# Kernel optimization log

Hardware: AMD Instinct MI355X
Metric: run time of the kernel (lower is better)

The kernel has to match this reference:

```python
import jax, jax.numpy as jnp
import numpy as np

EPS = 1e-5
G = 8    # groups
K = 3    # kernel_size


def bn(x, gamma, beta, mean, var):
    # inference-mode BatchNorm2d; x: (b,C,H,W), params: (C,)
    inv = gamma / jnp.sqrt(var + EPS)
    return x * inv[None, :, None, None] + (beta - mean * inv)[None, :, None, None]


def gconv1x1(x, w):
    # grouped 1x1 conv; x: (b, g*ci, H, W), w: (g, co, ci) -> (b, g*co, H, W)
    b, C, H, W = x.shape
    g, co, ci = w.shape
    xg = x.reshape(b, g, ci, H, W)
    y = jnp.einsum('bgihw,goi->bgohw', xg, w)
    return y.reshape(b, g * co, H, W)


def unfold3(x):
    # torch.nn.Unfold(k=3, stride=1, dilation=1, padding=1), reshaped to (b, C, 9, H, W)
    b, C, H, W = x.shape
    xp = jnp.pad(x, ((0, 0), (0, 0), (1, 1), (1, 1)))
    patches = [xp[:, :, i:i + H, j:j + W] for i in range(K) for j in range(K)]
    return jnp.stack(patches, axis=2)


def setup_inputs() -> dict:
    key = jax.random.key(0)
    ks = jax.random.split(key, 16)
    f = jax.random.normal
    u = jax.random.uniform
    return {
        'x':  f(ks[0], (2, 256, 128, 128), jnp.float32),
        'w1': f(ks[1], (8, 8, 32), jnp.float32) * 0.1,
        'b1': f(ks[2], (64,), jnp.float32) * 0.1,
        'g1': u(ks[3], (64,), jnp.float32, 0.5, 1.5),
        'be1': f(ks[4], (64,), jnp.float32) * 0.1,
        'm1': f(ks[5], (64,), jnp.float32) * 0.1,
        'v1': u(ks[6], (64,), jnp.float32, 0.5, 1.5),
        'w2': f(ks[7], (8, 10, 8), jnp.float32) * 0.1,
        'b2': f(ks[8], (80,), jnp.float32) * 0.1,
        'g2': u(ks[9], (80,), jnp.float32, 0.5, 1.5),
        'be2': f(ks[10], (80,), jnp.float32) * 0.1,
        'm2': f(ks[11], (80,), jnp.float32) * 0.1,
        'v2': u(ks[12], (80,), jnp.float32, 0.5, 1.5),
        'wv': f(ks[13], (8, 32, 32), jnp.float32) * 0.1,
    }


def reference(x, w1, b1, g1, be1, m1, v1, w2, b2, g2, be2, m2, v2, wv):
    b, C, H, W = x.shape
    # mask_conv: grouped 1x1 conv -> BN -> tanh -> grouped 1x1 conv -> BN
    t = jnp.tanh(bn(gconv1x1(x, w1) + b1[None, :, None, None], g1, be1, m1, v1))
    mn = bn(gconv1x1(t, w2) + b2[None, :, None, None], g2, be2, m2, v2)  # (b, G*(1+K*K), H, W)
    neighbor = mn[:, :G]          # (b, G, H, W)
    mask = mn[:, G:]              # (b, G*K*K, H, W)
    nb = unfold3(neighbor)        # (b, G, 9, H, W)
    logits = mask.reshape(b, G, K * K, H, W) + nb
    attn = jax.nn.softmax(logits, axis=2)               # (b, G, 9, H, W)
    # value path: grouped 1x1 conv (no bias) then unfold
    v = gconv1x1(x, wv)                                  # (b, C, H, W)
    vu = unfold3(v).reshape(b, G, C // G, K * K, H, W)   # (b, G, C/G, 9, H, W)
    out = jnp.einsum('bgkhw,bgckhw->bgchw', attn, vu)    # weighted sum over window
    return out.reshape(b, C, H, W)
```

## Files before the change

kernel.cpp:

```cpp
#include <hip/hip_runtime.h>

#define HW  16384
#define WD  128

#define TS   16
#define HS   18
#define HP   (HS * HS)
#define PRS  20
#define PLS  360

__device__ __forceinline__ unsigned short f2bf(float f) {
    unsigned int u = __builtin_bit_cast(unsigned int, f);
    u += 0x7FFFu + ((u >> 16) & 1u);
    return (unsigned short)(u >> 16);
}
__device__ __forceinline__ float bf2f(unsigned int s) {
    return __builtin_bit_cast(float, (s & 0xFFFFu) << 16);
}
__device__ __forceinline__ float ftanh(float v) {
    const float e = __expf(2.0f * v);
    return 1.0f - __fdividef(2.0f, e + 1.0f);
}

__global__ __launch_bounds__(256) void la_t(
    const float* __restrict__ x,
    const float* __restrict__ w1, const float* __restrict__ b1,
    const float* __restrict__ g1, const float* __restrict__ be1,
    const float* __restrict__ m1, const float* __restrict__ v1,
    ushort4* __restrict__ t4, uint4* __restrict__ xbf)
{
    const int z   = blockIdx.x;
    const int b   = blockIdx.y;
    const int pix = blockIdx.z * blockDim.x + threadIdx.x;
    const int p   = z & 7;
    const int h   = z >> 3;

    const float* xp = x + (size_t)(b * 256 + p * 32) * HW + pix;
    float xv[32];
#pragma unroll
    for (int c = 0; c < 32; ++c) xv[c] = xp[(size_t)c * HW];

#pragma unroll
    for (int j = 0; j < 2; ++j) {
        const int c8 = h * 2 + j;
        uint4 u;
        u.x = (unsigned)f2bf(xv[c8 * 8 + 0]) | ((unsigned)f2bf(xv[c8 * 8 + 1]) << 16);
        u.y = (unsigned)f2bf(xv[c8 * 8 + 2]) | ((unsigned)f2bf(xv[c8 * 8 + 3]) << 16);
        u.z = (unsigned)f2bf(xv[c8 * 8 + 4]) | ((unsigned)f2bf(xv[c8 * 8 + 5]) << 16);
        u.w = (unsigned)f2bf(xv[c8 * 8 + 6]) | ((unsigned)f2bf(xv[c8 * 8 + 7]) << 16);
        xbf[((size_t)((b * 8 + p) * 4 + c8)) * HW + pix] = u;
    }

    const float* w1g = w1 + p * 256 + h * 4 * 32;
    float tv[4];
#pragma unroll
    for (int o = 0; o < 4; ++o) {
        float a = 0.f;
#pragma unroll
        for (int ci = 0; ci < 32; ++ci) a = fmaf(xv[ci], w1g[o * 32 + ci], a);
        const int ch = p * 8 + h * 4 + o;
        const float inv = g1[ch] * rsqrtf(v1[ch] + 1e-5f);
        const float add = be1[ch] + (b1[ch] - m1[ch]) * inv;
        tv[o] = ftanh(fmaf(a, inv, add));
    }

    t4[((size_t)((b * 8 + p) * 2 + h)) * HW + pix] =
        make_ushort4(f2bf(tv[0]), f2bf(tv[1]), f2bf(tv[2]), f2bf(tv[3]));
}

__global__ __launch_bounds__(256, 4) void la_fused(
    const float* __restrict__ w2, const float* __restrict__ b2,
    const float* __restrict__ g2, const float* __restrict__ be2,
    const float* __restrict__ m2, const float* __restrict__ v2,
    const float* __restrict__ wv,
    const ushort4* __restrict__ t4, const uint4* __restrict__ xbf,
    float* __restrict__ out)
{
    __shared__ uint4 xt[4 * PLS];
    __shared__ float nbs[PLS];

    const int tid  = threadIdx.x;
    const int bg   = blockIdx.x;
    const int tile = blockIdx.y;
    const int b    = bg >> 3, g = bg & 7;
    const int ty0  = (tile >> 3) * TS;
    const int tx0  = (tile & 7) * TS;

    const uint4*   xg = xbf + (size_t)((b * 8 + g) * 4) * HW;
    const ushort4* t0 = t4  + (size_t)(b * 16) * HW;

    const int cy  = tid >> 4, cx = tid & 15;
    const int ciy = ty0 + cy, cix = tx0 + cx;
    const int cpx = ciy * WD + cix;

    const int mc0    = 8 + 9 * g;
    const int pa     = mc0 / 10;
    const int pb     = (mc0 + 8) / 10;
    const int ksplit = 10 - (mc0 - pa * 10);

    const ushort4 tAlo = t4[((size_t)((b * 8 + pa) * 2 + 0)) * HW + cpx];
    const ushort4 tAhi = t4[((size_t)((b * 8 + pa) * 2 + 1)) * HW + cpx];
    const ushort4 tBlo = t4[((size_t)((b * 8 + pb) * 2 + 0)) * HW + cpx];
    const ushort4 tBhi = t4[((size_t)((b * 8 + pb) * 2 + 1)) * HW + cpx];

    const float inv2n = g2[g] * rsqrtf(v2[g] + 1e-5f);
    const float add2n = be2[g] + (b2[g] - m2[g]) * inv2n;

    for (int hp = tid; hp < HP; hp += 256) {
        const int hy = hp / HS, hx = hp - hy * HS;
        const int iy = ty0 + hy - 1, ix = tx0 + hx - 1;
        const int slot = hy * PRS + hx;
        if (((unsigned)iy < 128u) && ((unsigned)ix < 128u)) {
            const int po = iy * WD + ix;
            const ushort4 ta = t0[po];
            const ushort4 tb = t0[(size_t)HW + po];
            float an = 0.f;
            an = fmaf(bf2f(ta.x), w2[g * 8 + 0], an);
            an = fmaf(bf2f(ta.y), w2[g * 8 + 1], an);
            an = fmaf(bf2f(ta.z), w2[g * 8 + 2], an);
            an = fmaf(bf2f(ta.w), w2[g * 8 + 3], an);
            an = fmaf(bf2f(tb.x), w2[g * 8 + 4], an);
            an = fmaf(bf2f(tb.y), w2[g * 8 + 5], an);
            an = fmaf(bf2f(tb.z), w2[g * 8 + 6], an);
            an = fmaf(bf2f(tb.w), w2[g * 8 + 7], an);
            nbs[slot] = fmaf(an, inv2n, add2n);
#pragma unroll
            for (int c8 = 0; c8 < 4; ++c8)
                xt[c8 * PLS + slot] = xg[(size_t)c8 * HW + po];
        } else {
            const uint4 z = make_uint4(0u, 0u, 0u, 0u);
#pragma unroll
            for (int c8 = 0; c8 < 4; ++c8) xt[c8 * PLS + slot] = z;
            nbs[slot] = 0.f;
        }
    }
    __syncthreads();

    float tA[8], tB[8];
    tA[0] = bf2f(tAlo.x); tA[1] = bf2f(tAlo.y);
    tA[2] = bf2f(tAlo.z); tA[3] = bf2f(tAlo.w);
    tA[4] = bf2f(tAhi.x); tA[5] = bf2f(tAhi.y);
    tA[6] = bf2f(tAhi.z); tA[7] = bf2f(tAhi.w);
    tB[0] = bf2f(tBlo.x); tB[1] = bf2f(tBlo.y);
    tB[2] = bf2f(tBlo.z); tB[3] = bf2f(tBlo.w);
    tB[4] = bf2f(tBhi.x); tB[5] = bf2f(tBhi.y);
    tB[6] = bf2f(tBhi.z); tB[7] = bf2f(tBhi.w);

    float lg[9];
    float mx = -1e30f;
#pragma unroll
    for (int k = 0; k < 9; ++k) {
        const int mc = mc0 + k;
        const int p  = (k < ksplit) ? pa : pb;
        const int o  = mc - p * 10;
        const float* w2p = w2 + p * 80 + o * 8;
        float a = 0.f;
#pragma unroll
        for (int i = 0; i < 8; ++i) {
            const float ti = (k < ksplit) ? tA[i] : tB[i];
            a = fmaf(ti, w2p[i], a);
        }
        const float inv = g2[mc] * rsqrtf(v2[mc] + 1e-5f);
        const float add = be2[mc] + (b2[mc] - m2[mc]) * inv;
        lg[k] = fmaf(a, inv, add) + nbs[(cy + k / 3) * PRS + (cx + k % 3)];
        mx = fmaxf(mx, lg[k]);
    }
    float ssum = 0.f;
#pragma unroll
    for (int k = 0; k < 9; ++k) { lg[k] = __expf(lg[k] - mx); ssum += lg[k]; }
    const float rs = 1.f / ssum;

    float s[32];
#pragma unroll
    for (int c = 0; c < 32; ++c) s[c] = 0.f;
#pragma unroll
    for (int k = 0; k < 9; ++k) {
        const int slot = (cy + k / 3) * PRS + (cx + k % 3);
        const float e = lg[k];
#pragma unroll
        for (int c8 = 0; c8 < 4; ++c8) {
            const uint4 u = xt[c8 * PLS + slot];
            s[c8 * 8 + 0] = fmaf(e, bf2f(u.x),       s[c8 * 8 + 0]);
            s[c8 * 8 + 1] = fmaf(e, bf2f(u.x >> 16), s[c8 * 8 + 1]);
            s[c8 * 8 + 2] = fmaf(e, bf2f(u.y),       s[c8 * 8 + 2]);
            s[c8 * 8 + 3] = fmaf(e, bf2f(u.y >> 16), s[c8 * 8 + 3]);
            s[c8 * 8 + 4] = fmaf(e, bf2f(u.z),       s[c8 * 8 + 4]);
            s[c8 * 8 + 5] = fmaf(e, bf2f(u.z >> 16), s[c8 * 8 + 5]);
            s[c8 * 8 + 6] = fmaf(e, bf2f(u.w),       s[c8 * 8 + 6]);
            s[c8 * 8 + 7] = fmaf(e, bf2f(u.w >> 16), s[c8 * 8 + 7]);
        }
    }

    const float* wvg = wv + g * 1024;
    float* og = out + (size_t)(b * 256 + g * 32) * HW + cpx;
#pragma unroll 4
    for (int o = 0; o < 32; ++o) {
        const float* wp = wvg + o * 32;
        float a = 0.f;
#pragma unroll
        for (int ci = 0; ci < 32; ++ci) a = fmaf(s[ci], wp[ci], a);
        __builtin_nontemporal_store(a * rs, og + (size_t)o * HW);
    }
}

extern "C" void kernel_launch(void* const* d_in, const int* in_sizes, int n_in,
                              void* d_out, int out_size, void* d_ws, size_t ws_size,
                              hipStream_t stream)
{
    const float* x   = (const float*)d_in[0];
    const float* w1  = (const float*)d_in[1];
    const float* b1  = (const float*)d_in[2];
    const float* g1  = (const float*)d_in[3];
    const float* be1 = (const float*)d_in[4];
    const float* m1  = (const float*)d_in[5];
    const float* v1  = (const float*)d_in[6];
    const float* w2  = (const float*)d_in[7];
    const float* b2  = (const float*)d_in[8];
    const float* g2  = (const float*)d_in[9];
    const float* be2 = (const float*)d_in[10];
    const float* m2  = (const float*)d_in[11];
    const float* v2  = (const float*)d_in[12];
    const float* wv  = (const float*)d_in[13];

    float* out = (float*)d_out;
    ushort4* t4  = (ushort4*)d_ws;
    uint4*   xbf = (uint4*)((char*)d_ws + (size_t)32 * HW * 8);

    dim3 blk(256);
    dim3 gt(16, 2, HW / 256);
    dim3 gfd(16, 64);

    hipLaunchKernelGGL(la_t, gt, blk, 0, stream,
                       x, w1, b1, g1, be1, m1, v1, t4, xbf);
    hipLaunchKernelGGL(la_fused, gfd, blk, 0, stream,
                       w2, b2, g2, be2, m2, v2, wv, t4, xbf, out);
}
```

Before: 129.3 us.

## Compute value projection with bf16 MFMA via shared-memory staged aggregates

```diff
diff --git a/kernel.cpp b/kernel.cpp
--- a/kernel.cpp
+++ b/kernel.cpp
@@ -8,6 +8,10 @@
 #define HP   (HS * HS)
 #define PRS  20
 #define PLS  360
+#define SROW 80
+
+typedef __attribute__((ext_vector_type(8))) short bf16x8;
+typedef __attribute__((ext_vector_type(4))) float f32x4;
 
 __device__ __forceinline__ unsigned short f2bf(float f) {
     unsigned int u = __builtin_bit_cast(unsigned int, f);
@@ -68,7 +72,7 @@
         make_ushort4(f2bf(tv[0]), f2bf(tv[1]), f2bf(tv[2]), f2bf(tv[3]));
 }
 
-__global__ __launch_bounds__(256, 4) void la_fused(
+__global__ __launch_bounds__(256) void la_fused(
     const float* __restrict__ w2, const float* __restrict__ b2,
     const float* __restrict__ g2, const float* __restrict__ be2,
     const float* __restrict__ m2, const float* __restrict__ v2,
@@ -85,13 +89,24 @@
     const int b    = bg >> 3, g = bg & 7;
     const int ty0  = (tile >> 3) * TS;
     const int tx0  = (tile & 7) * TS;
+    const int lane = tid & 63, wv4 = tid >> 6;
 
     const uint4*   xg = xbf + (size_t)((b * 8 + g) * 4) * HW;
     const ushort4* t0 = t4  + (size_t)(b * 16) * HW;
 
+    const float* wvg = wv + g * 1024;
+    bf16x8 bfrag[2];
+#pragma unroll
+    for (int nt = 0; nt < 2; ++nt) {
+        const float* wp = wvg + (nt * 16 + (lane & 15)) * 32 + (lane >> 4) * 8;
+        bf16x8 f;
+#pragma unroll
+        for (int j = 0; j < 8; ++j) f[j] = (short)f2bf(wp[j]);
+        bfrag[nt] = f;
+    }
+
     const int cy  = tid >> 4, cx = tid & 15;
-    const int ciy = ty0 + cy, cix = tx0 + cx;
-    const int cpx = ciy * WD + cix;
+    const int cpx = (ty0 + cy) * WD + (tx0 + cx);
 
     const int mc0    = 8 + 9 * g;
     const int pa     = mc0 / 10;
@@ -191,15 +206,38 @@
         }
     }
 
-    const float* wvg = wv + g * 1024;
-    float* og = out + (size_t)(b * 256 + g * 32) * HW + cpx;
-#pragma unroll 4
-    for (int o = 0; o < 32; ++o) {
-        const float* wp = wvg + o * 32;
-        float a = 0.f;
-#pragma unroll
-        for (int ci = 0; ci < 32; ++ci) a = fmaf(s[ci], wp[ci], a);
-        __builtin_nontemporal_store(a * rs, og + (size_t)o * HW);
+    __syncthreads();
+    char* Sb = (char*)xt;
+    {
+        uint4* row = (uint4*)(Sb + tid * SROW);
+#pragma unroll
+        for (int q = 0; q < 4; ++q) {
+            uint4 u;
+            u.x = (unsigned)f2bf(rs * s[q * 8 + 0]) | ((unsigned)f2bf(rs * s[q * 8 + 1]) << 16);
+            u.y = (unsigned)f2bf(rs * s[q * 8 + 2]) | ((unsigned)f2bf(rs * s[q * 8 + 3]) << 16);
+            u.z = (unsigned)f2bf(rs * s[q * 8 + 4]) | ((unsigned)f2bf(rs * s[q * 8 + 5]) << 16);
+            u.w = (unsigned)f2bf(rs * s[q * 8 + 6]) | ((unsigned)f2bf(rs * s[q * 8 + 7]) << 16);
+            row[q] = u;
+        }
+    }
+    __syncthreads();
+
+    float* outg = out + (size_t)(b * 256 + g * 32) * HW;
+#pragma unroll
+    for (int t = 0; t < 4; ++t) {
+        const uint4 av = *(const uint4*)(Sb +
+            (wv4 * 64 + t * 16 + (lane & 15)) * SROW + (lane >> 4) * 16);
+        const bf16x8 af = __builtin_bit_cast(bf16x8, av);
+#pragma unroll
+        for (int nt = 0; nt < 2; ++nt) {
+            f32x4 c = {0.f, 0.f, 0.f, 0.f};
+            c = __builtin_amdgcn_mfma_f32_16x16x32_bf16(af, bfrag[nt], c, 0, 0, 0);
+            const int ch  = nt * 16 + (lane & 15);
+            const int idx = wv4 * 64 + t * 16 + 4 * (lane >> 4);
+            const int oy  = ty0 + (idx >> 4), ox = tx0 + (idx & 15);
+            f32x4* addr = (f32x4*)(outg + (size_t)ch * HW + oy * WD + ox);
+            __builtin_nontemporal_store(c, addr);
+        }
     }
 }
 
```

Result: faster. 124.3 us (-3.9%).
